# Optimization experiments

Hardware: AMD Instinct MI355X
Metric: run time of the kernel (lower is better)

## Reference

```python
import jax, jax.numpy as jnp
import numpy as np

NUM_HEADS = 12


def setup_inputs() -> dict:
    key = jax.random.key(0)
    ks = jax.random.split(key, 6)
    B, N, C = 2, 1569, 768  # N = 1 + num_frames * seq_len = 1 + 8*196
    s = 0.02
    return {
        "x": jax.random.normal(ks[0], (B, N, C), jnp.float32),
        "W_qkv": jax.random.normal(ks[1], (C, 3 * C), jnp.float32) * s,
        "W_pq": jax.random.normal(ks[2], (C, C), jnp.float32) * s,
        "W_pkv": jax.random.normal(ks[3], (C, 2 * C), jnp.float32) * s,
        "W_proj": jax.random.normal(ks[4], (C, C), jnp.float32) * s,
        "b_proj": jax.random.normal(ks[5], (C,), jnp.float32) * s,
        "seq_len": 196,
        "num_frames": 8,
    }


def reference(x, W_qkv, W_pq, W_pkv, W_proj, b_proj, seq_len, num_frames):
    h = NUM_HEADS
    B, N, C = x.shape
    d = C // h
    P, F = seq_len, num_frames  # N == 1 + F*P
    S = F * P
    scale = d ** (-0.5)

    # qkv projection (no bias), split heads -> (B*h, N, d)
    qkv = x @ W_qkv
    q, k, v = jnp.split(qkv, 3, axis=-1)

    def heads(t):
        return t.reshape(B, N, h, d).transpose(0, 2, 1, 3).reshape(B * h, N, d)

    q, k, v = map(heads, (q, k, v))

    # --- CLS token: plain attention over all tokens ---
    cls_sim = jnp.einsum('bid,bjd->bij', q[:, :1] * scale, k)  # (B*h,1,N)
    cls_attn = jax.nn.softmax(cls_sim, axis=-1)
    cls_out = jnp.einsum('bij,bjd->bid', cls_attn, v)  # (B*h,1,d)
    cls_out = cls_out.reshape(B, h, 1, d).transpose(0, 2, 1, 3).reshape(B, 1, C)

    # --- Stage 1: space attention (softmax over patches n within each frame f) ---
    q_, k_, v_ = q[:, 1:], k[:, 1:], v[:, 1:]  # (B*h, S, d)
    q_dot_k = jnp.einsum('bqd,bnd->bqn', q_, k_).reshape(B * h, S, F, P)
    space_attn = jax.nn.softmax(scale * q_dot_k, axis=-1)  # (B*h, S, F, P)
    v4 = v_.reshape(B * h, F, P, d)
    traj = jnp.einsum('bqfn,bfnd->bqfd', space_attn, v4)  # (B*h, S, F, d)
    # merge heads into channels: (B, S, F, C)
    traj = traj.reshape(B, h, S, F, d).transpose(0, 2, 3, 1, 4).reshape(B, S, F, C)

    # --- Diagonal gather: token s=f*P+n takes its own-frame trajectory f ---
    fidx = jnp.repeat(jnp.arange(F), P)  # (S,)
    x_diag = jnp.take_along_axis(traj, fidx[None, :, None, None], axis=2)[:, :, 0, :]  # (B,S,C)

    # --- Stage 2: temporal attention over frames f ---
    q2 = (x_diag @ W_pq).reshape(B, S, h, d).transpose(0, 2, 1, 3) * scale  # (B,h,S,d)
    kv2 = traj @ W_pkv  # (B,S,F,2C)
    k2, v2 = jnp.split(kv2, 2, axis=-1)

    def heads5(t):  # (B,S,F,C) -> (B,h,S,F,d)
        return t.reshape(B, S, F, h, d).transpose(0, 3, 1, 2, 4)

    k2 = heads5(k2)
    attn = jax.nn.softmax(jnp.einsum('bhsd,bhsfd->bhsf', q2, k2), axis=-1)  # (B,h,S,F)
    # use_original_code=True: values are the trajectory tensor itself, not v2
    xv = heads5(traj)
    out = jnp.einsum('bhsf,bhsfd->bhsd', attn, xv)  # (B,h,S,d)
    out = out.transpose(0, 2, 1, 3).reshape(B, S, C)

    out = jnp.concatenate([cls_out, out], axis=1) @ W_proj + b_proj  # (B,N,C)
    return out, attn
```

## Files before the change

kernel.cpp:

```cpp
#include <hip/hip_runtime.h>

#define B_ 2
#define N_ 1569
#define C_ 768
#define H_ 12
#define D_ 64
#define P_ 196
#define F_ 8
#define S_ 1568
#define QKVLD 2304
#define SCALE 0.125f

typedef unsigned short ushort_t;
using short8 = __attribute__((ext_vector_type(8))) short;
using f32x4  = __attribute__((ext_vector_type(4))) float;

__device__ __forceinline__ ushort_t f2bf(float x) {
    unsigned u = __float_as_uint(x);
    u += 0x7fffu + ((u >> 16) & 1);
    return (ushort_t)(u >> 16);
}
__device__ __forceinline__ float bf2f(ushort_t h) {
    return __uint_as_float((unsigned)h << 16);
}
__device__ __forceinline__ uint2 pack4(float a, float b, float c, float d) {
    uint2 o;
    o.x = f2bf(a) | ((unsigned)f2bf(b) << 16);
    o.y = f2bf(c) | ((unsigned)f2bf(d) << 16);
    return o;
}
__device__ __forceinline__ void gl2lds16(const void* g, void* l) {
    __builtin_amdgcn_global_load_lds(
        (const __attribute__((address_space(1))) unsigned int*)g,
        (__attribute__((address_space(3))) unsigned int*)l, 16, 0, 0);
}

__global__ __launch_bounds__(256)
void cvt_f32_bf16(const float* __restrict__ s, ushort_t* __restrict__ d, int n4)
{
    int i = blockIdx.x * 256 + threadIdx.x;
    if (i < n4) {
        float4 v = ((const float4*)s)[i];
        ((uint2*)d)[i] = pack4(v.x, v.y, v.z, v.w);
    }
}

__global__ __launch_bounds__(256)
void transpose_cvt(const float* __restrict__ src, ushort_t* __restrict__ dst,
                   int K, int ldsrc)
{
    __shared__ float tle[32][33];
    const int n0 = blockIdx.x * 32, k0 = blockIdx.y * 32;
    const int tx = threadIdx.x & 31, ty = threadIdx.x >> 5;
#pragma unroll
    for (int j = 0; j < 4; j++)
        tle[ty + 8 * j][tx] = src[(long)(k0 + ty + 8 * j) * ldsrc + n0 + tx];
    __syncthreads();
#pragma unroll
    for (int j = 0; j < 4; j++)
        dst[(long)(n0 + ty + 8 * j) * K + k0 + tx] = f2bf(tle[tx][ty + 8 * j]);
}

template<int GATHER, int OUTBF>
__global__ __launch_bounds__(256)
void gemm_bf16(const ushort_t* __restrict__ A, const ushort_t* __restrict__ Bt,
               void* __restrict__ Cv, int M, int Nn, int K,
               float alpha, const float* __restrict__ bias)
{
    __shared__ ushort_t As[2][128][32];
    __shared__ ushort_t Bs[2][128][32];

    const int tid = threadIdx.x;
    const int m0 = blockIdx.x * 128, n0 = blockIdx.y * 128;
    const int wave = tid >> 6, lane = tid & 63;
    const int wm = (wave & 1) * 64, wn = (wave >> 1) * 64;
    const int lrow = lane & 15, quad = lane >> 4;

    const int srow = tid >> 2, sseg = tid & 3;
    const int sw = sseg ^ ((srow >> 1) & 3);
    int ma0 = m0 + srow;      if (ma0 >= M) ma0 = M - 1;
    int ma1 = m0 + 64 + srow; if (ma1 >= M) ma1 = M - 1;
    long ra0, ra1;
    if (GATHER) {
        ra0 = (long)ma0 * F_ + (ma0 % S_) / P_;
        ra1 = (long)ma1 * F_ + (ma1 % S_) / P_;
    } else { ra0 = ma0; ra1 = ma1; }
    const ushort_t* ap0 = A + ra0 * K + sw * 8;
    const ushort_t* ap1 = A + ra1 * K + sw * 8;
    const ushort_t* bp0 = Bt + (long)(n0 + srow) * K + sw * 8;
    const ushort_t* bp1 = Bt + (long)(n0 + 64 + srow) * K + sw * 8;

    f32x4 acc[4][4];
#pragma unroll
    for (int i = 0; i < 4; i++)
#pragma unroll
        for (int j = 0; j < 4; j++) acc[i][j] = (f32x4){0.f, 0.f, 0.f, 0.f};

    gl2lds16(ap0, &As[0][srow][sseg * 8]);
    gl2lds16(ap1, &As[0][64 + srow][sseg * 8]);
    gl2lds16(bp0, &Bs[0][srow][sseg * 8]);
    gl2lds16(bp1, &Bs[0][64 + srow][sseg * 8]);

    const int csw = (quad ^ ((lrow >> 1) & 3)) * 8;

    const int nk = K >> 5;
    for (int kt = 0; kt < nk; kt++) {
        const int cur = kt & 1, nxt = cur ^ 1;
        __syncthreads();
        if (kt + 1 < nk) {
            const int k1 = (kt + 1) * 32;
            gl2lds16(ap0 + k1, &As[nxt][srow][sseg * 8]);
            gl2lds16(ap1 + k1, &As[nxt][64 + srow][sseg * 8]);
            gl2lds16(bp0 + k1, &Bs[nxt][srow][sseg * 8]);
            gl2lds16(bp1 + k1, &Bs[nxt][64 + srow][sseg * 8]);
        }
        short8 af[4], bf[4];
#pragma unroll
        for (int mt = 0; mt < 4; mt++)
            af[mt] = *(const short8*)&As[cur][wm + mt * 16 + lrow][csw];
#pragma unroll
        for (int nt = 0; nt < 4; nt++)
            bf[nt] = *(const short8*)&Bs[cur][wn + nt * 16 + lrow][csw];
#pragma unroll
        for (int mt = 0; mt < 4; mt++)
#pragma unroll
            for (int nt = 0; nt < 4; nt++)
                acc[mt][nt] = __builtin_amdgcn_mfma_f32_16x16x32_bf16(
                    af[mt], bf[nt], acc[mt][nt], 0, 0, 0);
    }

#pragma unroll
    for (int mt = 0; mt < 4; mt++) {
#pragma unroll
        for (int nt = 0; nt < 4; nt++) {
            int row = m0 + wm + mt * 16 + quad * 4;
            int col = n0 + wn + nt * 16 + lrow;
            float bv = bias ? bias[col] : 0.f;
#pragma unroll
            for (int r = 0; r < 4; r++) {
                if (row + r < M) {
                    float v = acc[mt][nt][r] * alpha + bv;
                    if (OUTBF)
                        ((ushort_t*)Cv)[(long)(row + r) * Nn + col] = f2bf(v);
                    else
                        ((float*)Cv)[(long)(row + r) * Nn + col] = v;
                }
            }
        }
    }
}

__global__ __launch_bounds__(256)
void prep_kv(const float* __restrict__ qkv, ushort_t* __restrict__ q_bf,
             ushort_t* __restrict__ k_bf, ushort_t* __restrict__ vT_bf)
{
    const int f = blockIdx.x, h = blockIdx.y, b = blockIdx.z;
    const int t = threadIdx.x;
    const long rowbase = (long)(b * N_ + 1 + f * P_) * QKVLD;

    {
        ushort_t* qd = q_bf + ((long)(b * H_ + h) * S_ + f * P_) * 64;
        for (int u = t; u < P_ * 16; u += 256) {
            int row = u >> 4, seg = u & 15;
            float4 v = *(const float4*)(qkv + rowbase + (long)row * QKVLD + h * 64 + seg * 4);
            *(uint2*)(qd + (long)row * 64 + seg * 4) = pack4(v.x, v.y, v.z, v.w);
        }
    }
    {
        ushort_t* kd = k_bf + (long)((b * H_ + h) * F_ + f) * 13312;
        for (int u = t; u < 208 * 16; u += 256) {
            int key = u >> 4, seg = u & 15;
            float4 v = make_float4(0.f, 0.f, 0.f, 0.f);
            if (key < P_)
                v = *(const float4*)(qkv + rowbase + (long)key * QKVLD + 768 + h * 64 + seg * 4);
            int ks = seg >> 3, qq = (seg >> 1) & 3, j0 = (seg & 1) * 4;
            int nt = key >> 4, lr = key & 15;
            *(uint2*)(kd + ((ks * 13 + nt) * 64 + qq * 16 + lr) * 8 + j0)
                = pack4(v.x, v.y, v.z, v.w);
        }
    }
    __shared__ float Vl[224][68];
    for (int u = t; u < 224 * 16; u += 256) {
        int key = u >> 4, seg = u & 15;
        float4 v = make_float4(0.f, 0.f, 0.f, 0.f);
        if (key < P_)
            v = *(const float4*)(qkv + rowbase + (long)key * QKVLD + 1536 + h * 64 + seg * 4);
        *(float4*)&Vl[key][seg * 4] = v;
    }
    __syncthreads();
    {
        ushort_t* vd = vT_bf + (long)((b * H_ + h) * F_ + f) * 14336;
        for (int u = t; u < 64 * 56; u += 256) {
            int d = u / 56, kb = u % 56;
            int s = kb >> 3, qq = (kb >> 1) & 3, j0 = (kb & 1) * 4;
            int nt = d >> 4, lr = d & 15;
            *(uint2*)(vd + ((s * 4 + nt) * 64 + qq * 16 + lr) * 8 + j0) =
                pack4(Vl[kb*4+0][d], Vl[kb*4+1][d], Vl[kb*4+2][d], Vl[kb*4+3][d]);
        }
    }
}

__global__ __launch_bounds__(256)
void traj_attn_mfma(const ushort_t* __restrict__ q_bf,
                    const ushort_t* __restrict__ k_bf,
                    const ushort_t* __restrict__ vT_bf,
                    ushort_t* __restrict__ traj)
{
    __shared__ __align__(16) ushort_t Pl[4][7 * 512];

    const int t = threadIdx.x;
    const int wave = t >> 6, lane = t & 63;
    const int lrow = lane & 15, quad = lane >> 4;
    const int qt = blockIdx.x, h = blockIdx.y, b = blockIdx.z;
    const int s0 = qt * 64;
    const bool v12 = (lrow < 4);

    int qrow = s0 + wave * 16 + lrow; if (qrow > S_ - 1) qrow = S_ - 1;
    const ushort_t* qp = q_bf + ((long)(b * H_ + h) * S_ + qrow) * 64 + quad * 8;
    short8 a0 = *(const short8*)qp;
    short8 a1 = *(const short8*)(qp + 32);

    *(uint2*)&Pl[wave][6 * 512 + 256 + lane * 4] = (uint2){0, 0};

    const ushort_t* kfb = k_bf  + (long)((b * H_ + h) * F_) * 13312;
    const ushort_t* vfb = vT_bf + (long)((b * H_ + h) * F_) * 14336;

#pragma unroll 1
    for (int f = 0; f < F_; f++) {
        const ushort_t* kf = kfb + (long)f * 13312;
        const ushort_t* vf = vfb + (long)f * 14336;

        f32x4 acc[13];
#pragma unroll
        for (int nt = 0; nt < 13; nt++) acc[nt] = (f32x4){0.f, 0.f, 0.f, 0.f};
#pragma unroll
        for (int nt = 0; nt < 13; nt++) {
            short8 bv = *(const short8*)(kf + (long)nt * 512 + lane * 8);
            acc[nt] = __builtin_amdgcn_mfma_f32_16x16x32_bf16(a0, bv, acc[nt], 0, 0, 0);
        }
#pragma unroll
        for (int nt = 0; nt < 13; nt++) {
            short8 bv = *(const short8*)(kf + (long)(13 + nt) * 512 + lane * 8);
            acc[nt] = __builtin_amdgcn_mfma_f32_16x16x32_bf16(a1, bv, acc[nt], 0, 0, 0);
        }

        float rl[4];
#pragma unroll
        for (int r = 0; r < 4; r++) {
            float mx = acc[0][r];
#pragma unroll
            for (int nt = 1; nt < 12; nt++) mx = fmaxf(mx, acc[nt][r]);
            if (v12) mx = fmaxf(mx, acc[12][r]);
#pragma unroll
            for (int off = 1; off < 16; off <<= 1)
                mx = fmaxf(mx, __shfl_xor(mx, off, 16));
            float sum = 0.f;
#pragma unroll
            for (int nt = 0; nt < 12; nt++) {
                float w = __expf((acc[nt][r] - mx) * SCALE);
                acc[nt][r] = w; sum += w;
            }
            {
                float w = v12 ? __expf((acc[12][r] - mx) * SCALE) : 0.f;
                acc[12][r] = w; sum += w;
            }
#pragma unroll
            for (int off = 1; off < 16; off <<= 1)
                sum += __shfl_xor(sum, off, 16);
            rl[r] = 1.f / sum;
        }

#pragma unroll
        for (int nt = 0; nt < 13; nt++) {
            int key = nt * 16 + lrow;
            int base = (key >> 5) * 512 + ((key >> 3) & 3) * 128 + (key & 7) + quad * 32;
#pragma unroll
            for (int r = 0; r < 4; r++)
                Pl[wave][base + r * 8] = f2bf(acc[nt][r]);
        }
        asm volatile("s_waitcnt lgkmcnt(0)" ::: "memory");

        f32x4 av[4];
#pragma unroll
        for (int nt = 0; nt < 4; nt++) av[nt] = (f32x4){0.f, 0.f, 0.f, 0.f};
#pragma unroll
        for (int s = 0; s < 7; s++) {
            short8 af = *(const short8*)&Pl[wave][s * 512 + lane * 8];
#pragma unroll
            for (int nt = 0; nt < 4; nt++) {
                short8 bv = *(const short8*)(vf + (long)(s * 4 + nt) * 512 + lane * 8);
                av[nt] = __builtin_amdgcn_mfma_f32_16x16x32_bf16(af, bv, av[nt], 0, 0, 0);
            }
        }

#pragma unroll
        for (int nt = 0; nt < 4; nt++)
#pragma unroll
            for (int r = 0; r < 4; r++) {
                int so = s0 + wave * 16 + quad * 4 + r;
                if (so < S_)
                    traj[((long)(b * S_ + so) * F_ + f) * C_ + h * 64 + nt * 16 + lrow]
                        = f2bf(av[nt][r] * rl[r]);
            }
    }
}

#define CLS_CH 13
__global__ __launch_bounds__(256)
void cls_attn_part(const float* __restrict__ qkv, float* __restrict__ part)
{
    const int c = blockIdx.x, hh = blockIdx.y, b = blockIdx.z;
    const int t = threadIdx.x;
    const int n0 = c * 128;
    const int nk = (N_ - n0 < 128) ? (N_ - n0) : 128;

    __shared__ float qs[64];
    __shared__ float sc[128];
    __shared__ float red[256];

    if (t < 64) qs[t] = qkv[(long)(b * N_) * QKVLD + hh * 64 + t];
    __syncthreads();

    if (t < 128) {
        float acc = -1e30f;
        if (t < nk) {
            const float* krow = qkv + (long)(b * N_ + n0 + t) * QKVLD + 768 + hh * 64;
            acc = 0.f;
#pragma unroll
            for (int j4 = 0; j4 < 16; j4++) {
                float4 kv = *(const float4*)(krow + j4 * 4);
                acc = fmaf(kv.x, qs[j4*4+0], acc);
                acc = fmaf(kv.y, qs[j4*4+1], acc);
                acc = fmaf(kv.z, qs[j4*4+2], acc);
                acc = fmaf(kv.w, qs[j4*4+3], acc);
            }
            acc *= SCALE;
        }
        sc[t] = acc;
        red[t] = acc;
    }
    __syncthreads();
    for (int s = 64; s > 0; s >>= 1) {
        if (t < s && t + s < 128) red[t] = fmaxf(red[t], red[t + s]);
        __syncthreads();
    }
    const float m = red[0];
    __syncthreads();

    if (t < 128) {
        float w = (t < nk) ? __expf(sc[t] - m) : 0.f;
        sc[t] = w;
        red[t] = w;
    }
    __syncthreads();
    for (int s = 64; s > 0; s >>= 1) {
        if (t < s && t + s < 128) red[t] += red[t + s];
        __syncthreads();
    }
    const float lsum = red[0];
    __syncthreads();

    const int j = t & 63, grp = t >> 6;
    float acc = 0.f;
    for (int n = grp; n < nk; n += 4)
        acc = fmaf(sc[n], qkv[(long)(b * N_ + n0 + n) * QKVLD + 1536 + hh * 64 + j], acc);
    red[t] = acc;
    __syncthreads();

    float* pp = part + (long)(((b * H_ + hh) * CLS_CH) + c) * 68;
    if (t < 64)
        pp[2 + t] = red[t] + red[64 + t] + red[128 + t] + red[192 + t];
    if (t == 0) { pp[0] = m; pp[1] = lsum; }
}

__global__ __launch_bounds__(64)
void cls_attn_merge(const float* __restrict__ part, float* __restrict__ outcat)
{
    const int bh = blockIdx.x;
    const int b = bh / H_, hh = bh % H_;
    const int t = threadIdx.x;
    const float* pp = part + (long)(bh * CLS_CH) * 68;

    float m = -1e30f;
#pragma unroll
    for (int c = 0; c < CLS_CH; c++) m = fmaxf(m, pp[c * 68]);
    float l = 0.f, o = 0.f;
#pragma unroll
    for (int c = 0; c < CLS_CH; c++) {
        float w = __expf(pp[c * 68] - m);
        l = fmaf(pp[c * 68 + 1], w, l);
        o = fmaf(pp[c * 68 + 2 + t], w, o);
    }
    outcat[(long)(b * N_) * C_ + hh * 64 + t] = o / l;
}

__global__ __launch_bounds__(256)
void attn2_kernel(const float* __restrict__ q2, const ushort_t* __restrict__ k2,
                  const ushort_t* __restrict__ traj, float* __restrict__ outcat,
                  float* __restrict__ attn_out)
{
    const int bs = blockIdx.x;
    const int b = bs / S_, s = bs % S_;
    __shared__ float qs[768];
    __shared__ ushort_t ks[8 * 768];
    __shared__ float logit[12][8];
    __shared__ float wsm[12][8];
    const int t = threadIdx.x;

    const float* qrow = q2 + (long)bs * 768;
    if (t < 192) *(float4*)&qs[t * 4] = *(const float4*)(qrow + t * 4);
    const uint4* krow = (const uint4*)(k2 + (long)bs * 6144);
#pragma unroll
    for (int u = t; u < 768; u += 256)
        *(uint4*)&ks[u * 8] = krow[u];
    __syncthreads();

    if (t < 96) {
        int hh = t >> 3, f = t & 7;
        float acc = 0.f;
#pragma unroll 8
        for (int j = 0; j < 64; j++)
            acc = fmaf(qs[hh * 64 + j], bf2f(ks[f * 768 + hh * 64 + j]), acc);
        logit[hh][f] = acc;
    }
    __syncthreads();
    if (t < 12) {
        float m = logit[t][0];
#pragma unroll
        for (int f = 1; f < 8; f++) m = fmaxf(m, logit[t][f]);
        float w[8], sum = 0.f;
#pragma unroll
        for (int f = 0; f < 8; f++) { w[f] = __expf(logit[t][f] - m); sum += w[f]; }
        float r = 1.f / sum;
#pragma unroll
        for (int f = 0; f < 8; f++) wsm[t][f] = w[f] * r;
    }
    __syncthreads();
    if (t < 96) {
        int hh = t >> 3, f = t & 7;
        attn_out[((long)(b * H_ + hh) * S_ + s) * 8 + f] = wsm[hh][f];
    }
    if (t < 96) {
        const int c0 = t * 8, hh = t >> 3;
        const ushort_t* trow = traj + (long)bs * 6144;
        float o[8];
#pragma unroll
        for (int i = 0; i < 8; i++) o[i] = 0.f;
#pragma unroll
        for (int f = 0; f < 8; f++) {
            uint4 tv = *(const uint4*)(trow + f * 768 + c0);
            float wv = wsm[hh][f];
            const ushort_t* e = (const ushort_t*)&tv;
#pragma unroll
            for (int i = 0; i < 8; i++) o[i] = fmaf(wv, bf2f(e[i]), o[i]);
        }
        float* orow = outcat + ((long)(b * N_) + 1 + s) * 768 + c0;
        *(float4*)orow       = make_float4(o[0], o[1], o[2], o[3]);
        *(float4*)(orow + 4) = make_float4(o[4], o[5], o[6], o[7]);
    }
}

extern "C" void kernel_launch(void* const* d_in, const int* in_sizes, int n_in,
                              void* d_out, int out_size, void* d_ws, size_t ws_size,
                              hipStream_t stream)
{
    (void)in_sizes; (void)n_in; (void)out_size; (void)ws_size;
    const float* x     = (const float*)d_in[0];
    const float* Wqkv  = (const float*)d_in[1];
    const float* Wpq   = (const float*)d_in[2];
    const float* Wpkv  = (const float*)d_in[3];
    const float* Wproj = (const float*)d_in[4];
    const float* bproj = (const float*)d_in[5];
    float* out = (float*)d_out;

    char* p = (char*)d_ws;
    float*    qkv     = (float*)p;
    ushort_t* traj_bf = (ushort_t*)p;
    p += (size_t)25088 * 768 * 2;
    float* q2 = (float*)p;  p += (size_t)3136 * 768 * 4;
    char* c0 = p;
    ushort_t* k2_bf = (ushort_t*)c0;
    ushort_t* x_bf  = (ushort_t*)c0;
    ushort_t* q_bf  = (ushort_t*)(c0 + (size_t)4819968);
    ushort_t* k_bf  = (ushort_t*)(c0 + (size_t)4819968 + 4816896);
    ushort_t* vT_bf = (ushort_t*)(c0 + (size_t)4819968 + 4816896 + 5111808);
    p += (size_t)25088 * 768 * 2;
    float*    outcat    = (float*)p;     p += (size_t)3138 * 768 * 4;
    ushort_t* outcat_bf = (ushort_t*)p;  p += (size_t)3138 * 768 * 2;
    ushort_t* Wqkv_t  = (ushort_t*)p;    p += (size_t)1769472 * 2;
    ushort_t* Wpq_t   = (ushort_t*)p;    p += (size_t)589824 * 2;
    ushort_t* Wpkv_t  = (ushort_t*)p;    p += (size_t)589824 * 2;
    ushort_t* Wproj_t = (ushort_t*)p;    p += (size_t)589824 * 2;
    float*    cls_part = (float*)p;      p += (size_t)24 * CLS_CH * 68 * 4;
    float* attn_out = out + (size_t)3138 * 768;

    cvt_f32_bf16<<<2354, 256, 0, stream>>>(x, x_bf, 602496);
    transpose_cvt<<<dim3(72, 24), 256, 0, stream>>>(Wqkv,  Wqkv_t,  768, 2304);
    transpose_cvt<<<dim3(24, 24), 256, 0, stream>>>(Wpq,   Wpq_t,   768, 768);
    transpose_cvt<<<dim3(24, 24), 256, 0, stream>>>(Wpkv,  Wpkv_t,  768, 1536);
    transpose_cvt<<<dim3(24, 24), 256, 0, stream>>>(Wproj, Wproj_t, 768, 768);

    gemm_bf16<0, 0><<<dim3(25, 18), 256, 0, stream>>>(x_bf, Wqkv_t, qkv, 3138, 2304, 768, 1.f, nullptr);
    prep_kv<<<dim3(8, 12, 2), 256, 0, stream>>>(qkv, q_bf, k_bf, vT_bf);
    cls_attn_part<<<dim3(CLS_CH, 12, 2), 256, 0, stream>>>(qkv, cls_part);
    cls_attn_merge<<<24, 64, 0, stream>>>(cls_part, outcat);
    traj_attn_mfma<<<dim3(25, 12, 2), 256, 0, stream>>>(q_bf, k_bf, vT_bf, traj_bf);
    gemm_bf16<1, 0><<<dim3(25, 6), 256, 0, stream>>>(traj_bf, Wpq_t, q2, 3136, 768, 768, SCALE, nullptr);
    gemm_bf16<0, 1><<<dim3(196, 6), 256, 0, stream>>>(traj_bf, Wpkv_t, k2_bf, 25088, 768, 768, 1.f, nullptr);
    attn2_kernel<<<3136, 256, 0, stream>>>(q2, k2_bf, traj_bf, outcat, attn_out);
    cvt_f32_bf16<<<2354, 256, 0, stream>>>(outcat, outcat_bf, 602496);
    gemm_bf16<0, 0><<<dim3(25, 6), 256, 0, stream>>>(outcat_bf, Wproj_t, out, 3138, 768, 768, 1.f, bproj);
}
```

Before: 348.6 us.

## Reassociate temporal logits to skip the K2 projection GEMM

The code no longer materializes k2 = traj @ W_pk for all frames. A new kernel computes u = q2 · W_pk^T per head with MFMA, then dots u against each frame's trajectory row to get the logits. It also fuses the softmax and the weighted sum over traj. This removes the large 25088x768x768 GEMM and its k2 write and read. In exchange it adds an LDS-staged intermediate rounded to bf16, and q2 is now stored in bf16, which may cost some accuracy.

```diff
diff --git a/kernel.cpp b/kernel.cpp
--- a/kernel.cpp
+++ b/kernel.cpp
@@ -42,6 +42,17 @@
     if (i < n4) {
         float4 v = ((const float4*)s)[i];
         ((uint2*)d)[i] = pack4(v.x, v.y, v.z, v.w);
+    }
+}
+
+__global__ __launch_bounds__(256)
+void cvt_pkv(const float* __restrict__ src, ushort_t* __restrict__ dst)
+{
+    int i = blockIdx.x * 256 + threadIdx.x;
+    if (i < 147456) {
+        int row = i / 192, c4 = (i % 192) * 4;
+        float4 v = *(const float4*)(src + (long)row * 1536 + c4);
+        *(uint2*)(dst + (long)row * 768 + c4) = pack4(v.x, v.y, v.z, v.w);
     }
 }
 
@@ -395,66 +406,109 @@
 }
 
 __global__ __launch_bounds__(256)
-void attn2_kernel(const float* __restrict__ q2, const ushort_t* __restrict__ k2,
-                  const ushort_t* __restrict__ traj, float* __restrict__ outcat,
-                  float* __restrict__ attn_out)
-{
-    const int bs = blockIdx.x;
-    const int b = bs / S_, s = bs % S_;
-    __shared__ float qs[768];
-    __shared__ ushort_t ks[8 * 768];
-    __shared__ float logit[12][8];
-    __shared__ float wsm[12][8];
+void logit_ws(const ushort_t* __restrict__ q2b, const ushort_t* __restrict__ wpk,
+              const ushort_t* __restrict__ traj, float* __restrict__ attn_out,
+              float* __restrict__ outcat)
+{
+    __shared__ ushort_t Ul[32 * 776];
+    __shared__ float wsm[32][8];
+
+    const int flat = blockIdx.x;
+    const int g = flat / 96, rr_ = flat % 96;
+    const int stile = g * 8 + (rr_ & 7);
+    const int h = rr_ >> 3;
+    if (stile >= 98) return;
+    const int b = stile / 49, st = stile % 49;
+    const int s0 = st * 32;
+
     const int t = threadIdx.x;
-
-    const float* qrow = q2 + (long)bs * 768;
-    if (t < 192) *(float4*)&qs[t * 4] = *(const float4*)(qrow + t * 4);
-    const uint4* krow = (const uint4*)(k2 + (long)bs * 6144);
-#pragma unroll
-    for (int u = t; u < 768; u += 256)
-        *(uint4*)&ks[u * 8] = krow[u];
-    __syncthreads();
-
-    if (t < 96) {
-        int hh = t >> 3, f = t & 7;
-        float acc = 0.f;
-#pragma unroll 8
-        for (int j = 0; j < 64; j++)
-            acc = fmaf(qs[hh * 64 + j], bf2f(ks[f * 768 + hh * 64 + j]), acc);
-        logit[hh][f] = acc;
-    }
-    __syncthreads();
-    if (t < 12) {
-        float m = logit[t][0];
-#pragma unroll
-        for (int f = 1; f < 8; f++) m = fmaxf(m, logit[t][f]);
-        float w[8], sum = 0.f;
-#pragma unroll
-        for (int f = 0; f < 8; f++) { w[f] = __expf(logit[t][f] - m); sum += w[f]; }
-        float r = 1.f / sum;
-#pragma unroll
-        for (int f = 0; f < 8; f++) wsm[t][f] = w[f] * r;
-    }
-    __syncthreads();
-    if (t < 96) {
-        int hh = t >> 3, f = t & 7;
-        attn_out[((long)(b * H_ + hh) * S_ + s) * 8 + f] = wsm[hh][f];
-    }
-    if (t < 96) {
-        const int c0 = t * 8, hh = t >> 3;
-        const ushort_t* trow = traj + (long)bs * 6144;
+    const int wave = t >> 6, lane = t & 63;
+    const int lrow = lane & 15, quad = lane >> 4;
+
+    f32x4 acc[2][12];
+#pragma unroll
+    for (int mt = 0; mt < 2; mt++)
+#pragma unroll
+        for (int nt = 0; nt < 12; nt++) acc[mt][nt] = (f32x4){0.f, 0.f, 0.f, 0.f};
+
+    short8 afr[2][2];
+    {
+        const ushort_t* qbase = q2b + (long)(b * S_ + s0) * 768 + h * 64;
+#pragma unroll
+        for (int mt = 0; mt < 2; mt++)
+#pragma unroll
+            for (int ks = 0; ks < 2; ks++)
+                afr[mt][ks] = *(const short8*)(qbase + (long)(mt * 16 + lrow) * 768
+                                               + ks * 32 + quad * 8);
+    }
+    {
+        const ushort_t* wbase = wpk + (long)(wave * 192 + lrow) * 768 + h * 64;
+#pragma unroll
+        for (int ks = 0; ks < 2; ks++)
+#pragma unroll
+            for (int nt = 0; nt < 12; nt++) {
+                short8 bfr = *(const short8*)(wbase + (long)nt * 16 * 768
+                                              + ks * 32 + quad * 8);
+                acc[0][nt] = __builtin_amdgcn_mfma_f32_16x16x32_bf16(
+                    afr[0][ks], bfr, acc[0][nt], 0, 0, 0);
+                acc[1][nt] = __builtin_amdgcn_mfma_f32_16x16x32_bf16(
+                    afr[1][ks], bfr, acc[1][nt], 0, 0, 0);
+            }
+    }
+#pragma unroll
+    for (int mt = 0; mt < 2; mt++)
+#pragma unroll
+        for (int nt = 0; nt < 12; nt++)
+#pragma unroll
+            for (int r = 0; r < 4; r++)
+                Ul[(mt * 16 + quad * 4 + r) * 776 + wave * 192 + nt * 16 + lrow]
+                    = f2bf(acc[mt][nt][r]);
+    __syncthreads();
+
+    const int ss = t >> 3, f = t & 7;
+    {
+        const ushort_t* trow = traj + ((long)(b * S_ + s0 + ss) * F_ + f) * 768;
+        float dot = 0.f;
+#pragma unroll 4
+        for (int c0 = 0; c0 < 768; c0 += 8) {
+            uint4 tv = *(const uint4*)(trow + c0);
+            uint4 uv = *(const uint4*)&Ul[ss * 776 + c0];
+            const ushort_t* te = (const ushort_t*)&tv;
+            const ushort_t* ue = (const ushort_t*)&uv;
+#pragma unroll
+            for (int i = 0; i < 8; i++)
+                dot = fmaf(bf2f(te[i]), bf2f(ue[i]), dot);
+        }
+        float mx = dot;
+        mx = fmaxf(mx, __shfl_xor(mx, 1, 8));
+        mx = fmaxf(mx, __shfl_xor(mx, 2, 8));
+        mx = fmaxf(mx, __shfl_xor(mx, 4, 8));
+        float e = __expf(dot - mx);
+        float sum = e;
+        sum += __shfl_xor(sum, 1, 8);
+        sum += __shfl_xor(sum, 2, 8);
+        sum += __shfl_xor(sum, 4, 8);
+        float w = e / sum;
+        wsm[ss][f] = w;
+        attn_out[(((long)b * H_ + h) * S_ + s0 + ss) * 8 + f] = w;
+    }
+    __syncthreads();
+
+    {
+        const int c8 = (t & 7) * 8;
+        const ushort_t* tr2 = traj + ((long)(b * S_ + s0 + ss) * F_) * 768 + h * 64 + c8;
         float o[8];
 #pragma unroll
         for (int i = 0; i < 8; i++) o[i] = 0.f;
 #pragma unroll
-        for (int f = 0; f < 8; f++) {
-            uint4 tv = *(const uint4*)(trow + f * 768 + c0);
-            float wv = wsm[hh][f];
+        for (int f2 = 0; f2 < 8; f2++) {
+            uint4 tv = *(const uint4*)(tr2 + (long)f2 * 768);
+            float wv = wsm[ss][f2];
             const ushort_t* e = (const ushort_t*)&tv;
 #pragma unroll
             for (int i = 0; i < 8; i++) o[i] = fmaf(wv, bf2f(e[i]), o[i]);
         }
-        float* orow = outcat + ((long)(b * N_) + 1 + s) * 768 + c0;
+        float* orow = outcat + ((long)(b * N_) + 1 + s0 + ss) * 768 + h * 64 + c8;
         *(float4*)orow       = make_float4(o[0], o[1], o[2], o[3]);
         *(float4*)(orow + 4) = make_float4(o[4], o[5], o[6], o[7]);
     }
@@ -477,9 +531,8 @@
     float*    qkv     = (float*)p;
     ushort_t* traj_bf = (ushort_t*)p;
     p += (size_t)25088 * 768 * 2;
-    float* q2 = (float*)p;  p += (size_t)3136 * 768 * 4;
+    ushort_t* q2_bf = (ushort_t*)p;  p += (size_t)3136 * 768 * 2;
     char* c0 = p;
-    ushort_t* k2_bf = (ushort_t*)c0;
     ushort_t* x_bf  = (ushort_t*)c0;
     ushort_t* q_bf  = (ushort_t*)(c0 + (size_t)4819968);
     ushort_t* k_bf  = (ushort_t*)(c0 + (size_t)4819968 + 4816896);
@@ -489,7 +542,7 @@
     ushort_t* outcat_bf = (ushort_t*)p;  p += (size_t)3138 * 768 * 2;
     ushort_t* Wqkv_t  = (ushort_t*)p;    p += (size_t)1769472 * 2;
     ushort_t* Wpq_t   = (ushort_t*)p;    p += (size_t)589824 * 2;
-    ushort_t* Wpkv_t  = (ushort_t*)p;    p += (size_t)589824 * 2;
+    ushort_t* Wpkv_bf = (ushort_t*)p;    p += (size_t)589824 * 2;
     ushort_t* Wproj_t = (ushort_t*)p;    p += (size_t)589824 * 2;
     float*    cls_part = (float*)p;      p += (size_t)24 * CLS_CH * 68 * 4;
     float* attn_out = out + (size_t)3138 * 768;
@@ -497,7 +550,7 @@
     cvt_f32_bf16<<<2354, 256, 0, stream>>>(x, x_bf, 602496);
     transpose_cvt<<<dim3(72, 24), 256, 0, stream>>>(Wqkv,  Wqkv_t,  768, 2304);
     transpose_cvt<<<dim3(24, 24), 256, 0, stream>>>(Wpq,   Wpq_t,   768, 768);
-    transpose_cvt<<<dim3(24, 24), 256, 0, stream>>>(Wpkv,  Wpkv_t,  768, 1536);
+    cvt_pkv<<<576, 256, 0, stream>>>(Wpkv, Wpkv_bf);
     transpose_cvt<<<dim3(24, 24), 256, 0, stream>>>(Wproj, Wproj_t, 768, 768);
 
     gemm_bf16<0, 0><<<dim3(25, 18), 256, 0, stream>>>(x_bf, Wqkv_t, qkv, 3138, 2304, 768, 1.f, nullptr);
@@ -505,9 +558,8 @@
     cls_attn_part<<<dim3(CLS_CH, 12, 2), 256, 0, stream>>>(qkv, cls_part);
     cls_attn_merge<<<24, 64, 0, stream>>>(cls_part, outcat);
     traj_attn_mfma<<<dim3(25, 12, 2), 256, 0, stream>>>(q_bf, k_bf, vT_bf, traj_bf);
-    gemm_bf16<1, 0><<<dim3(25, 6), 256, 0, stream>>>(traj_bf, Wpq_t, q2, 3136, 768, 768, SCALE, nullptr);
-    gemm_bf16<0, 1><<<dim3(196, 6), 256, 0, stream>>>(traj_bf, Wpkv_t, k2_bf, 25088, 768, 768, 1.f, nullptr);
-    attn2_kernel<<<3136, 256, 0, stream>>>(q2, k2_bf, traj_bf, outcat, attn_out);
+    gemm_bf16<1, 1><<<dim3(25, 6), 256, 0, stream>>>(traj_bf, Wpq_t, q2_bf, 3136, 768, 768, SCALE, nullptr);
+    logit_ws<<<1248, 256, 0, stream>>>(q2_bf, Wpkv_bf, traj_bf, attn_out, outcat);
     cvt_f32_bf16<<<2354, 256, 0, stream>>>(outcat, outcat_bf, 602496);
     gemm_bf16<0, 0><<<dim3(25, 6), 256, 0, stream>>>(outcat_bf, Wproj_t, out, 3138, 768, 768, 1.f, bproj);
 }
```

Result: no change. 354.0 us (+1.5%).
